# Kernel optimization log

Measured on AMD Instinct MI355X. Metric: run time of the kernel, lower is better.

The kernel has to match this reference:

```python
import jax, jax.numpy as jnp
import numpy as np

N_NODES = 50000
N_EDGES = 600000
HIDDEN = 128


def _sage_conv(x, src, dst, W_l, W_r, b):
    """PyG SAGEConv with mean aggregation:
    out_i = W_l @ mean_{j in N(i)} x_j + W_r @ x_i + b
    src/dst: [E] edge endpoints (message flows src -> dst).
    """
    msg = x[src]  # [E, d] gather
    agg = jax.ops.segment_sum(msg, dst, num_segments=N_NODES)  # [N, d]
    cnt = jax.ops.segment_sum(jnp.ones((src.shape[0],), x.dtype), dst,
                              num_segments=N_NODES)  # [N]
    mean = agg / jnp.maximum(cnt, 1.0)[:, None]
    return mean @ W_l.T + x @ W_r.T + b


def setup_inputs() -> dict:
    key = jax.random.key(0)
    ks = jax.random.split(key, 12)
    x = jax.random.normal(ks[0], (N_NODES, HIDDEN), dtype=jnp.float32)
    edge_index = jax.random.randint(ks[1], (2, N_EDGES), 0, N_NODES, dtype=jnp.int64)
    scale = 1.0 / np.sqrt(HIDDEN)
    inp = {"x": x, "edge_index": edge_index}
    for i, layer in enumerate(["1", "2", "3"]):
        inp["Wl" + layer] = jax.random.uniform(ks[2 + 3 * i], (HIDDEN, HIDDEN),
                                               minval=-scale, maxval=scale, dtype=jnp.float32)
        inp["Wr" + layer] = jax.random.uniform(ks[3 + 3 * i], (HIDDEN, HIDDEN),
                                               minval=-scale, maxval=scale, dtype=jnp.float32)
        inp["b" + layer] = jax.random.uniform(ks[4 + 3 * i], (HIDDEN,),
                                              minval=-scale, maxval=scale, dtype=jnp.float32)
    return inp


def reference(x, edge_index, Wl1, Wr1, b1, Wl2, Wr2, b2, Wl3, Wr3, b3):
    src, dst = edge_index[0], edge_index[1]
    h = jax.nn.relu(_sage_conv(x, src, dst, Wl1, Wr1, b1))
    h = _sage_conv(h, src, dst, Wl2, Wr2, b2)
    h = _sage_conv(h, src, dst, Wl3, Wr3, b3)
    return h
```

## Files before the change

### kernel.cpp

```cpp
#include <hip/hip_runtime.h>
#include <hip/hip_bf16.h>

#define N_NODES 50000
#define N_EDGES 600000
#define HID 128

typedef __attribute__((ext_vector_type(8))) short s8v;
typedef __attribute__((ext_vector_type(4))) float f4v;

__device__ __forceinline__ unsigned short f2bf(float x) {
    unsigned u = __float_as_uint(x);
    unsigned r = u + 0x7FFFu + ((u >> 16) & 1u);
    return (unsigned short)(r >> 16);
}
__device__ __forceinline__ float bf2f(unsigned short u) {
    return __uint_as_float((unsigned)u << 16);
}
__device__ __forceinline__ void split_bf(float x, unsigned short& hi, unsigned short& lo) {
    hi = f2bf(x);
    lo = f2bf(x - bf2f(hi));
}

__global__ void detect_mode(const void* __restrict__ edges, int* __restrict__ flag) {
    __shared__ int any;
    if (threadIdx.x == 0) any = 0;
    __syncthreads();
    const int* p = (const int*)edges;
    if (p[2 * threadIdx.x + 1] != 0) any = 1;
    __syncthreads();
    if (threadIdx.x == 0) *flag = (any == 0) ? 1 : 0;
}

__device__ __forceinline__ int edge_at(const void* edges, int mode64, long long idx) {
    return mode64 ? (int)((const long long*)edges)[idx] : ((const int*)edges)[idx];
}

__global__ void count_deg(const void* __restrict__ edges, const int* __restrict__ flag,
                          int* __restrict__ deg) {
    int e = blockIdx.x * 256 + threadIdx.x;
    if (e >= N_EDGES) return;
    int m = *flag;
    int d = edge_at(edges, m, (long long)N_EDGES + e);
    if ((unsigned)d < (unsigned)N_NODES) atomicAdd(&deg[d], 1);
}

__global__ void scan_block(const int* __restrict__ deg, int* __restrict__ offs,
                           int* __restrict__ blocksum) {
    __shared__ int sm[256];
    int i = blockIdx.x * 256 + threadIdx.x;
    int v = (i < N_NODES) ? deg[i] : 0;
    sm[threadIdx.x] = v;
    __syncthreads();
    #pragma unroll
    for (int s = 1; s < 256; s <<= 1) {
        int t = (threadIdx.x >= (unsigned)s) ? sm[threadIdx.x - s] : 0;
        __syncthreads();
        sm[threadIdx.x] += t;
        __syncthreads();
    }
    if (i < N_NODES) offs[i] = sm[threadIdx.x] - v;
    if (threadIdx.x == 255) blocksum[blockIdx.x] = sm[255];
}

__global__ void scan_top(int* __restrict__ blocksum, int nblocks) {
    __shared__ int sm[256];
    int v = ((int)threadIdx.x < nblocks) ? blocksum[threadIdx.x] : 0;
    sm[threadIdx.x] = v;
    __syncthreads();
    #pragma unroll
    for (int s = 1; s < 256; s <<= 1) {
        int t = (threadIdx.x >= (unsigned)s) ? sm[threadIdx.x - s] : 0;
        __syncthreads();
        sm[threadIdx.x] += t;
        __syncthreads();
    }
    if ((int)threadIdx.x < nblocks) blocksum[threadIdx.x] = sm[threadIdx.x] - v;
    if (threadIdx.x == 255) blocksum[nblocks] = sm[255];
}

__global__ void scan_add(int* __restrict__ offs, int* __restrict__ cursor,
                         const int* __restrict__ blocksum, int nblocks) {
    int i = blockIdx.x * 256 + threadIdx.x;
    if (i < N_NODES) {
        int o = offs[i] + blocksum[blockIdx.x];
        offs[i] = o;
        cursor[i] = o;
    }
    if (i == 0) offs[N_NODES] = blocksum[nblocks];
}

__global__ void fill_csr(const void* __restrict__ edges, const int* __restrict__ flag,
                         int* __restrict__ cursor, int* __restrict__ csr) {
    int e = blockIdx.x * 256 + threadIdx.x;
    if (e >= N_EDGES) return;
    int m = *flag;
    int d = edge_at(edges, m, (long long)N_EDGES + e);
    int s = edge_at(edges, m, (long long)e);
    if ((unsigned)d >= (unsigned)N_NODES || (unsigned)s >= (unsigned)N_NODES) return;
    int pos = atomicAdd(&cursor[d], 1);
    csr[pos] = s;
}

__global__ void convert_w(const float* __restrict__ m0, const float* __restrict__ m1,
                          const float* __restrict__ m2, const float* __restrict__ m3,
                          const float* __restrict__ m4, const float* __restrict__ m5,
                          unsigned short* __restrict__ whi, unsigned short* __restrict__ wlo) {
    int idx = blockIdx.x * 256 + threadIdx.x;
    if (idx >= 6 * HID * HID) return;
    int mat = idx >> 14, off = idx & 16383;
    const float* src = mat == 0 ? m0 : mat == 1 ? m1 : mat == 2 ? m2
                     : mat == 3 ? m3 : mat == 4 ? m4 : m5;
    unsigned short h, l;
    split_bf(src[off], h, l);
    whi[idx] = h; wlo[idx] = l;
}

__global__ void split_f32(const float* __restrict__ x, unsigned short* __restrict__ hi,
                          unsigned short* __restrict__ lo, int n4) {
    int i = blockIdx.x * 256 + threadIdx.x;
    if (i >= n4) return;
    float4 v = ((const float4*)x)[i];
    ushort4 h, l;
    split_bf(v.x, h.x, l.x);
    split_bf(v.y, h.y, l.y);
    split_bf(v.z, h.z, l.z);
    split_bf(v.w, h.w, l.w);
    ((ushort4*)hi)[i] = h;
    ((ushort4*)lo)[i] = l;
}

__global__ __launch_bounds__(256) void aggregate_bf16(const unsigned short* __restrict__ h,
                                                      const int* __restrict__ offs,
                                                      const int* __restrict__ csr,
                                                      unsigned short* __restrict__ mhi,
                                                      unsigned short* __restrict__ mlo) {
    int lane = threadIdx.x & 31;
    int node = blockIdx.x * 8 + (threadIdx.x >> 5);
    if (node >= N_NODES) return;
    int beg = offs[node], end = offs[node + 1];
    float a0 = 0.f, a1 = 0.f, a2 = 0.f, a3 = 0.f;
    int p = beg;
    for (; p + 4 <= end; p += 4) {
        int s0 = csr[p], s1 = csr[p + 1], s2 = csr[p + 2], s3 = csr[p + 3];
        ushort4 v0 = ((const ushort4*)(h + (size_t)s0 * HID))[lane];
        ushort4 v1 = ((const ushort4*)(h + (size_t)s1 * HID))[lane];
        ushort4 v2 = ((const ushort4*)(h + (size_t)s2 * HID))[lane];
        ushort4 v3 = ((const ushort4*)(h + (size_t)s3 * HID))[lane];
        a0 += (bf2f(v0.x) + bf2f(v1.x)) + (bf2f(v2.x) + bf2f(v3.x));
        a1 += (bf2f(v0.y) + bf2f(v1.y)) + (bf2f(v2.y) + bf2f(v3.y));
        a2 += (bf2f(v0.z) + bf2f(v1.z)) + (bf2f(v2.z) + bf2f(v3.z));
        a3 += (bf2f(v0.w) + bf2f(v1.w)) + (bf2f(v2.w) + bf2f(v3.w));
    }
    for (; p < end; ++p) {
        int s = csr[p];
        ushort4 v = ((const ushort4*)(h + (size_t)s * HID))[lane];
        a0 += bf2f(v.x); a1 += bf2f(v.y); a2 += bf2f(v.z); a3 += bf2f(v.w);
    }
    float inv = 1.0f / fmaxf((float)(end - beg), 1.0f);
    a0 *= inv; a1 *= inv; a2 *= inv; a3 *= inv;
    ushort4 hh, ll;
    split_bf(a0, hh.x, ll.x);
    split_bf(a1, hh.y, ll.y);
    split_bf(a2, hh.z, ll.z);
    split_bf(a3, hh.w, ll.w);
    ((ushort4*)(mhi + (size_t)node * HID))[lane] = hh;
    ((ushort4*)(mlo + (size_t)node * HID))[lane] = ll;
}

template <int RELU, int FINAL>
__global__ __launch_bounds__(256, 2) void sage_mfma(
    const unsigned short* __restrict__ Mhi, const unsigned short* __restrict__ Mlo,
    const unsigned short* __restrict__ Hhi, const unsigned short* __restrict__ Hlo,
    const unsigned short* __restrict__ Whi, const unsigned short* __restrict__ Wlo,
    const float* __restrict__ bias,
    unsigned short* __restrict__ ohi, unsigned short* __restrict__ olo,
    float* __restrict__ of32) {
    const int tid = threadIdx.x;
    const int wave = tid >> 6, lane = tid & 63;
    const int mIdx = lane & 15, q = lane >> 4;
    const int wrow = (wave & 1) * 64, wcol = (wave >> 1) * 64;
    const int rowBase = blockIdx.x * 128;

    size_t aoff[4], boff[4];
    #pragma unroll
    for (int t = 0; t < 4; ++t) {
        int node = rowBase + wrow + t * 16 + mIdx;
        if (node > N_NODES - 1) node = N_NODES - 1;
        aoff[t] = (size_t)node * HID + q * 8;
        boff[t] = (size_t)(wcol + t * 16 + mIdx) * HID + q * 8;
    }

    f4v acc[4][4];
    #pragma unroll
    for (int a = 0; a < 4; ++a)
        #pragma unroll
        for (int b = 0; b < 4; ++b) acc[a][b] = (f4v){0.f, 0.f, 0.f, 0.f};

    s8v Ah[2][4], Al[2][4], Bh[2][4], Bl[2][4];

    auto load = [&](int i, int buf) {
        const unsigned short* ah_ = (i < 4) ? Mhi : Hhi;
        const unsigned short* al_ = (i < 4) ? Mlo : Hlo;
        const int kc = (i & 3) * 32;
        const int wb = (i < 4) ? 0 : HID * HID;
        #pragma unroll
        for (int t = 0; t < 4; ++t) {
            Ah[buf][t] = *(const s8v*)(ah_ + aoff[t] + kc);
            Al[buf][t] = *(const s8v*)(al_ + aoff[t] + kc);
            Bh[buf][t] = *(const s8v*)(Whi + wb + boff[t] + kc);
            Bl[buf][t] = *(const s8v*)(Wlo + wb + boff[t] + kc);
        }
    };
    auto compute = [&](int buf) {
        #pragma unroll
        for (int mt = 0; mt < 4; ++mt)
            #pragma unroll
            for (int nt = 0; nt < 4; ++nt) {
                acc[mt][nt] = __builtin_amdgcn_mfma_f32_16x16x32_bf16(
                    Ah[buf][mt], Bh[buf][nt], acc[mt][nt], 0, 0, 0);
                acc[mt][nt] = __builtin_amdgcn_mfma_f32_16x16x32_bf16(
                    Al[buf][mt], Bh[buf][nt], acc[mt][nt], 0, 0, 0);
                acc[mt][nt] = __builtin_amdgcn_mfma_f32_16x16x32_bf16(
                    Ah[buf][mt], Bl[buf][nt], acc[mt][nt], 0, 0, 0);
            }
    };

    load(0, 0);
    #pragma unroll
    for (int i = 0; i < 8; ++i) {
        if (i < 7) load(i + 1, (i + 1) & 1);
        compute(i & 1);
    }

    float bv[4];
    #pragma unroll
    for (int nt = 0; nt < 4; ++nt) bv[nt] = bias[wcol + nt * 16 + mIdx];

    #pragma unroll
    for (int mt = 0; mt < 4; ++mt)
        #pragma unroll
        for (int r = 0; r < 4; ++r) {
            int node = rowBase + wrow + mt * 16 + q * 4 + r;
            if (node < N_NODES) {
                #pragma unroll
                for (int nt = 0; nt < 4; ++nt) {
                    int feat = wcol + nt * 16 + mIdx;
                    float v = acc[mt][nt][r] + bv[nt];
                    if (RELU) v = fmaxf(v, 0.f);
                    size_t oidx = (size_t)node * HID + feat;
                    if (FINAL) {
                        of32[oidx] = v;
                    } else {
                        unsigned short hh, ll;
                        split_bf(v, hh, ll);
                        ohi[oidx] = hh;
                        olo[oidx] = ll;
                    }
                }
            }
        }
}

extern "C" void kernel_launch(void* const* d_in, const int* in_sizes, int n_in,
                              void* d_out, int out_size, void* d_ws, size_t ws_size,
                              hipStream_t stream) {
    const float* x   = (const float*)d_in[0];
    const void* edges = d_in[1];
    const float* Wl1 = (const float*)d_in[2];
    const float* Wr1 = (const float*)d_in[3];
    const float* b1  = (const float*)d_in[4];
    const float* Wl2 = (const float*)d_in[5];
    const float* Wr2 = (const float*)d_in[6];
    const float* b2  = (const float*)d_in[7];
    const float* Wl3 = (const float*)d_in[8];
    const float* Wr3 = (const float*)d_in[9];
    const float* b3  = (const float*)d_in[10];
    float* out = (float*)d_out;

    char* ws = (char*)d_ws;
    size_t off = 0;
    auto alloc = [&](size_t bytes) -> void* {
        void* p = (void*)(ws + off);
        off += (bytes + 255) & ~(size_t)255;
        return p;
    };
    typedef unsigned short u16;
    const size_t FEAT = (size_t)N_NODES * HID;
    int* flag     = (int*)alloc(256);
    int* deg      = (int*)alloc((size_t)N_NODES * 4);
    int* offs     = (int*)alloc((size_t)(N_NODES + 1) * 4);
    int* cursor   = (int*)alloc((size_t)N_NODES * 4);
    int* blocksum = (int*)alloc(256 * 4);
    int* csr      = (int*)alloc((size_t)N_EDGES * 4);
    u16* whi      = (u16*)alloc((size_t)6 * HID * HID * 2);
    u16* wlo      = (u16*)alloc((size_t)6 * HID * HID * 2);
    u16* xhi      = (u16*)alloc(FEAT * 2);
    u16* xlo      = (u16*)alloc(FEAT * 2);
    u16* h1hi     = (u16*)alloc(FEAT * 2);
    u16* h1lo     = (u16*)alloc(FEAT * 2);
    u16* mhi      = (u16*)alloc(FEAT * 2);
    u16* mlo      = (u16*)alloc(FEAT * 2);
    (void)ws_size; (void)in_sizes; (void)n_in; (void)out_size;

    const int EB = (N_EDGES + 255) / 256;
    const int NB = (N_NODES + 255) / 256;
    const int AGG_B = (N_NODES + 7) / 8;
    const int GEMM_B = (N_NODES + 127) / 128;
    const int WCV_B = (6 * HID * HID + 255) / 256;
    const int XSP_B = ((int)(FEAT / 4) + 255) / 256;

    hipMemsetAsync(deg, 0, (size_t)N_NODES * 4, stream);
    detect_mode<<<1, 1024, 0, stream>>>(edges, flag);
    count_deg<<<EB, 256, 0, stream>>>(edges, flag, deg);
    scan_block<<<NB, 256, 0, stream>>>(deg, offs, blocksum);
    scan_top<<<1, 256, 0, stream>>>(blocksum, NB);
    scan_add<<<NB, 256, 0, stream>>>(offs, cursor, blocksum, NB);
    fill_csr<<<EB, 256, 0, stream>>>(edges, flag, cursor, csr);

    convert_w<<<WCV_B, 256, 0, stream>>>(Wl1, Wr1, Wl2, Wr2, Wl3, Wr3, whi, wlo);
    split_f32<<<XSP_B, 256, 0, stream>>>(x, xhi, xlo, (int)(FEAT / 4));

    aggregate_bf16<<<AGG_B, 256, 0, stream>>>(xhi, offs, csr, mhi, mlo);
    sage_mfma<1, 0><<<GEMM_B, 256, 0, stream>>>(mhi, mlo, xhi, xlo,
        whi, wlo, b1, h1hi, h1lo, (float*)nullptr);
    aggregate_bf16<<<AGG_B, 256, 0, stream>>>(h1hi, offs, csr, mhi, mlo);
    sage_mfma<0, 0><<<GEMM_B, 256, 0, stream>>>(mhi, mlo, h1hi, h1lo,
        whi + 2 * HID * HID, wlo + 2 * HID * HID, b2, xhi, xlo, (float*)nullptr);
    aggregate_bf16<<<AGG_B, 256, 0, stream>>>(xhi, offs, csr, mhi, mlo);
    sage_mfma<0, 1><<<GEMM_B, 256, 0, stream>>>(mhi, mlo, xhi, xlo,
        whi + 4 * HID * HID, wlo + 4 * HID * HID, b3,
        (u16*)nullptr, (u16*)nullptr, out);
}
```

Before: 356.0 us.

## Stage weight panels in LDS for MFMA GEMM and widen aggregation loads

The aggregation kernel now assigns 16 lanes per node, each loading 8 bf16 values (16 bytes) per neighbor, and unrolls over 8 neighbors to raise memory-level parallelism. The fused SAGE GEMM now stages each 128x64 weight panel (hi and lo parts) into padded shared memory, cooperatively loaded per block, instead of every wave reading weight fragments directly from global memory. This adds block-wide syncs and shared-memory use, and drops the occupancy hint from the launch bounds, which could change register allocation.

```diff
diff --git a/kernel.cpp b/kernel.cpp
--- a/kernel.cpp
+++ b/kernel.cpp
@@ -6,6 +6,7 @@
 #define HID 128
 
 typedef __attribute__((ext_vector_type(8))) short s8v;
+typedef __attribute__((ext_vector_type(8))) unsigned short u8v;
 typedef __attribute__((ext_vector_type(4))) float f4v;
 
 __device__ __forceinline__ unsigned short f2bf(float x) {
@@ -134,61 +135,83 @@
                                                       const int* __restrict__ csr,
                                                       unsigned short* __restrict__ mhi,
                                                       unsigned short* __restrict__ mlo) {
-    int lane = threadIdx.x & 31;
-    int node = blockIdx.x * 8 + (threadIdx.x >> 5);
+    const int sub  = threadIdx.x & 15;
+    const int node = blockIdx.x * 16 + (threadIdx.x >> 4);
     if (node >= N_NODES) return;
-    int beg = offs[node], end = offs[node + 1];
-    float a0 = 0.f, a1 = 0.f, a2 = 0.f, a3 = 0.f;
+    const int beg = offs[node], end = offs[node + 1];
+    float a[8] = {0.f, 0.f, 0.f, 0.f, 0.f, 0.f, 0.f, 0.f};
     int p = beg;
-    for (; p + 4 <= end; p += 4) {
+    for (; p + 8 <= end; p += 8) {
+        int s0 = csr[p],     s1 = csr[p + 1], s2 = csr[p + 2], s3 = csr[p + 3];
+        int s4 = csr[p + 4], s5 = csr[p + 5], s6 = csr[p + 6], s7 = csr[p + 7];
+        u8v v0 = *(const u8v*)(h + (size_t)s0 * HID + sub * 8);
+        u8v v1 = *(const u8v*)(h + (size_t)s1 * HID + sub * 8);
+        u8v v2 = *(const u8v*)(h + (size_t)s2 * HID + sub * 8);
+        u8v v3 = *(const u8v*)(h + (size_t)s3 * HID + sub * 8);
+        u8v v4 = *(const u8v*)(h + (size_t)s4 * HID + sub * 8);
+        u8v v5 = *(const u8v*)(h + (size_t)s5 * HID + sub * 8);
+        u8v v6 = *(const u8v*)(h + (size_t)s6 * HID + sub * 8);
+        u8v v7 = *(const u8v*)(h + (size_t)s7 * HID + sub * 8);
+        #pragma unroll
+        for (int j = 0; j < 8; ++j)
+            a[j] += ((bf2f(v0[j]) + bf2f(v1[j])) + (bf2f(v2[j]) + bf2f(v3[j])))
+                  + ((bf2f(v4[j]) + bf2f(v5[j])) + (bf2f(v6[j]) + bf2f(v7[j])));
+    }
+    if (p + 4 <= end) {
         int s0 = csr[p], s1 = csr[p + 1], s2 = csr[p + 2], s3 = csr[p + 3];
-        ushort4 v0 = ((const ushort4*)(h + (size_t)s0 * HID))[lane];
-        ushort4 v1 = ((const ushort4*)(h + (size_t)s1 * HID))[lane];
-        ushort4 v2 = ((const ushort4*)(h + (size_t)s2 * HID))[lane];
-        ushort4 v3 = ((const ushort4*)(h + (size_t)s3 * HID))[lane];
-        a0 += (bf2f(v0.x) + bf2f(v1.x)) + (bf2f(v2.x) + bf2f(v3.x));
-        a1 += (bf2f(v0.y) + bf2f(v1.y)) + (bf2f(v2.y) + bf2f(v3.y));
-        a2 += (bf2f(v0.z) + bf2f(v1.z)) + (bf2f(v2.z) + bf2f(v3.z));
-        a3 += (bf2f(v0.w) + bf2f(v1.w)) + (bf2f(v2.w) + bf2f(v3.w));
+        u8v v0 = *(const u8v*)(h + (size_t)s0 * HID + sub * 8);
+        u8v v1 = *(const u8v*)(h + (size_t)s1 * HID + sub * 8);
+        u8v v2 = *(const u8v*)(h + (size_t)s2 * HID + sub * 8);
+        u8v v3 = *(const u8v*)(h + (size_t)s3 * HID + sub * 8);
+        #pragma unroll
+        for (int j = 0; j < 8; ++j)
+            a[j] += (bf2f(v0[j]) + bf2f(v1[j])) + (bf2f(v2[j]) + bf2f(v3[j]));
+        p += 4;
     }
     for (; p < end; ++p) {
         int s = csr[p];
-        ushort4 v = ((const ushort4*)(h + (size_t)s * HID))[lane];
-        a0 += bf2f(v.x); a1 += bf2f(v.y); a2 += bf2f(v.z); a3 += bf2f(v.w);
-    }
-    float inv = 1.0f / fmaxf((float)(end - beg), 1.0f);
-    a0 *= inv; a1 *= inv; a2 *= inv; a3 *= inv;
-    ushort4 hh, ll;
-    split_bf(a0, hh.x, ll.x);
-    split_bf(a1, hh.y, ll.y);
-    split_bf(a2, hh.z, ll.z);
-    split_bf(a3, hh.w, ll.w);
-    ((ushort4*)(mhi + (size_t)node * HID))[lane] = hh;
-    ((ushort4*)(mlo + (size_t)node * HID))[lane] = ll;
+        u8v v = *(const u8v*)(h + (size_t)s * HID + sub * 8);
+        #pragma unroll
+        for (int j = 0; j < 8; ++j) a[j] += bf2f(v[j]);
+    }
+    const float inv = 1.0f / fmaxf((float)(end - beg), 1.0f);
+    u8v hh, ll;
+    #pragma unroll
+    for (int j = 0; j < 8; ++j) {
+        unsigned short hj, lj;
+        split_bf(a[j] * inv, hj, lj);
+        hh[j] = hj; ll[j] = lj;
+    }
+    *(u8v*)(mhi + (size_t)node * HID + sub * 8) = hh;
+    *(u8v*)(mlo + (size_t)node * HID + sub * 8) = ll;
 }
 
 template <int RELU, int FINAL>
-__global__ __launch_bounds__(256, 2) void sage_mfma(
+__global__ __launch_bounds__(256) void sage_mfma(
     const unsigned short* __restrict__ Mhi, const unsigned short* __restrict__ Mlo,
     const unsigned short* __restrict__ Hhi, const unsigned short* __restrict__ Hlo,
     const unsigned short* __restrict__ Whi, const unsigned short* __restrict__ Wlo,
     const float* __restrict__ bias,
     unsigned short* __restrict__ ohi, unsigned short* __restrict__ olo,
     float* __restrict__ of32) {
+    __shared__ short BhS[128 * 72];
+    __shared__ short BlS[128 * 72];
     const int tid = threadIdx.x;
     const int wave = tid >> 6, lane = tid & 63;
     const int mIdx = lane & 15, q = lane >> 4;
     const int wrow = (wave & 1) * 64, wcol = (wave >> 1) * 64;
     const int rowBase = blockIdx.x * 128;
 
-    size_t aoff[4], boff[4];
+    size_t aoff[4];
     #pragma unroll
     for (int t = 0; t < 4; ++t) {
         int node = rowBase + wrow + t * 16 + mIdx;
         if (node > N_NODES - 1) node = N_NODES - 1;
         aoff[t] = (size_t)node * HID + q * 8;
-        boff[t] = (size_t)(wcol + t * 16 + mIdx) * HID + q * 8;
-    }
+    }
+
+    const int bcol = tid & 127;
+    const int bseg = (tid >> 7) * 32;
 
     f4v acc[4][4];
     #pragma unroll
@@ -196,40 +219,62 @@
         #pragma unroll
         for (int b = 0; b < 4; ++b) acc[a][b] = (f4v){0.f, 0.f, 0.f, 0.f};
 
-    s8v Ah[2][4], Al[2][4], Bh[2][4], Bl[2][4];
-
-    auto load = [&](int i, int buf) {
+    s8v Ah[2][4], Al[2][4];
+    auto loadA = [&](int i, int buf) {
         const unsigned short* ah_ = (i < 4) ? Mhi : Hhi;
         const unsigned short* al_ = (i < 4) ? Mlo : Hlo;
         const int kc = (i & 3) * 32;
-        const int wb = (i < 4) ? 0 : HID * HID;
         #pragma unroll
         for (int t = 0; t < 4; ++t) {
             Ah[buf][t] = *(const s8v*)(ah_ + aoff[t] + kc);
             Al[buf][t] = *(const s8v*)(al_ + aoff[t] + kc);
-            Bh[buf][t] = *(const s8v*)(Whi + wb + boff[t] + kc);
-            Bl[buf][t] = *(const s8v*)(Wlo + wb + boff[t] + kc);
         }
     };
-    auto compute = [&](int buf) {
-        #pragma unroll
-        for (int mt = 0; mt < 4; ++mt)
+
+    loadA(0, 0);
+    for (int panel = 0; panel < 4; ++panel) {
+        const int ph = panel >> 1;
+        const int kb = (panel & 1) * 64;
+        const unsigned short* Wh_ = Whi + ph * HID * HID;
+        const unsigned short* Wl_ = Wlo + ph * HID * HID;
+        __syncthreads();
+        {
+            const unsigned short* sh = Wh_ + bcol * HID + kb + bseg;
+            const unsigned short* sl = Wl_ + bcol * HID + kb + bseg;
+            short* dh = BhS + bcol * 72 + bseg;
+            short* dl = BlS + bcol * 72 + bseg;
+            #pragma unroll
+            for (int j = 0; j < 4; ++j) {
+                *(s8v*)(dh + j * 8) = *(const s8v*)(sh + j * 8);
+                *(s8v*)(dl + j * 8) = *(const s8v*)(sl + j * 8);
+            }
+        }
+        __syncthreads();
+        #pragma unroll
+        for (int c = 0; c < 2; ++c) {
+            const int i = panel * 2 + c;
+            if (i < 7) loadA(i + 1, (i + 1) & 1);
+            const int kc2 = c * 32;
+            s8v Bh_f[4], Bl_f[4];
             #pragma unroll
             for (int nt = 0; nt < 4; ++nt) {
-                acc[mt][nt] = __builtin_amdgcn_mfma_f32_16x16x32_bf16(
-                    Ah[buf][mt], Bh[buf][nt], acc[mt][nt], 0, 0, 0);
-                acc[mt][nt] = __builtin_amdgcn_mfma_f32_16x16x32_bf16(
-                    Al[buf][mt], Bh[buf][nt], acc[mt][nt], 0, 0, 0);
-                acc[mt][nt] = __builtin_amdgcn_mfma_f32_16x16x32_bf16(
-                    Ah[buf][mt], Bl[buf][nt], acc[mt][nt], 0, 0, 0);
+                const int a = (wcol + nt * 16 + mIdx) * 72 + kc2 + q * 8;
+                Bh_f[nt] = *(const s8v*)(BhS + a);
+                Bl_f[nt] = *(const s8v*)(BlS + a);
             }
-    };
-
-    load(0, 0);
-    #pragma unroll
-    for (int i = 0; i < 8; ++i) {
-        if (i < 7) load(i + 1, (i + 1) & 1);
-        compute(i & 1);
+            const int buf = i & 1;
+            #pragma unroll
+            for (int mt = 0; mt < 4; ++mt)
+                #pragma unroll
+                for (int nt = 0; nt < 4; ++nt) {
+                    acc[mt][nt] = __builtin_amdgcn_mfma_f32_16x16x32_bf16(
+                        Ah[buf][mt], Bh_f[nt], acc[mt][nt], 0, 0, 0);
+                    acc[mt][nt] = __builtin_amdgcn_mfma_f32_16x16x32_bf16(
+                        Al[buf][mt], Bh_f[nt], acc[mt][nt], 0, 0, 0);
+                    acc[mt][nt] = __builtin_amdgcn_mfma_f32_16x16x32_bf16(
+                        Ah[buf][mt], Bl_f[nt], acc[mt][nt], 0, 0, 0);
+                }
+        }
     }
 
     float bv[4];
@@ -304,7 +349,7 @@
 
     const int EB = (N_EDGES + 255) / 256;
     const int NB = (N_NODES + 255) / 256;
-    const int AGG_B = (N_NODES + 7) / 8;
+    const int AGG_B = (N_NODES + 15) / 16;
     const int GEMM_B = (N_NODES + 127) / 128;
     const int WCV_B = (6 * HID * HID + 255) / 256;
     const int XSP_B = ((int)(FEAT / 4) + 255) / 256;
```

Result: faster. 340.7 us (-4.3%).
